# Optimization experiments

Measured on AMD Instinct MI355X. Metric: run time of the kernel, lower is better.

Reference implementation:

```python
import jax, jax.numpy as jnp
import numpy as np

B = 500000  # batch rows


def setup_inputs() -> dict:
    key = jax.random.key(0)
    k_x, k_v1, k_v2, k_l1, k_l2, k_l3 = jax.random.split(key, 6)
    return {
        "x": jax.random.normal(k_x, (B, 2), dtype=jnp.float32),
        "varphi1": jax.random.normal(k_v1, (300, 3), dtype=jnp.float32) * 0.1,
        "varphi2": jax.random.normal(k_v2, (1, 300), dtype=jnp.float32) * 0.1,
        "l1_diag": jax.random.normal(k_l1, (3,), dtype=jnp.float32),
        "l2_diag": jax.random.normal(k_l2, (300,), dtype=jnp.float32),
        "l3_diag": jax.random.normal(k_l3, (1,), dtype=jnp.float32),
    }


def reference(x, varphi1, varphi2, l1_diag, l2_diag, l3_diag):
    # append bias column of ones: [B, 3]
    xa = jnp.concatenate([x, jnp.ones((x.shape[0], 1), dtype=x.dtype)], axis=1)
    # diag(v) @ M == v[:, None] * M ; M @ diag(v) == M * v[None, :]
    W_21 = varphi1 * l1_diag[None, :] - l2_diag[:, None] * varphi1          # [300, 3]
    W_32 = varphi2 * l2_diag[None, :] - l3_diag[:, None] * varphi2          # [1, 300]
    W_31 = (l3_diag[:, None] * varphi2 - varphi2 * l2_diag[None, :]) @ varphi1  # [1, 3]
    # y = W_31 @ xa^T + W_32 @ relu(W_21 @ xa^T), returned transposed -> [B, 1]
    h = jax.nn.relu(xa @ W_21.T)                                            # [B, 300]
    y = xa @ W_31.T + h @ W_32.T                                            # [B, 1]
    return y
```

## Files before the change

kernel.cpp:

```cpp
#include <hip/hip_runtime.h>

#define NH   300
#define NPAD 320
#define BLK  256
#define RPT  8


__global__ __launch_bounds__(NPAD)
void phi2_precompute(const float* __restrict__ varphi1,
                     const float* __restrict__ varphi2,
                     const float* __restrict__ l1,
                     const float* __restrict__ l2,
                     const float* __restrict__ l3,
                     float4* __restrict__ coef,
                     float* __restrict__ w31p) {
    __shared__ float red[NPAD/64][3];
    int j = threadIdx.x;
    float p0 = 0.f, p1 = 0.f, p2 = 0.f;
    if (j < NH) {
        float lv2  = l2[j];
        float phi2 = varphi2[j];
        float W32  = phi2 * (lv2 - l3[0]);
        float s    = 0.5f * W32;
        float v0 = varphi1[j*3+0], v1 = varphi1[j*3+1], v2 = varphi1[j*3+2];
        float a = v0 * (l1[0] - lv2);
        float b = v1 * (l1[1] - lv2);
        float c = v2 * (l1[2] - lv2);
        float asafe = (fabsf(a) > 1e-20f) ? a : copysignf(1e-20f, a);
        coef[j] = make_float4(b / asafe, c / asafe, s * fabsf(asafe), 0.f);
        p0 = W32 * (0.5f * a - v0);
        p1 = W32 * (0.5f * b - v1);
        p2 = W32 * (0.5f * c - v2);
    } else {
        coef[j] = make_float4(0.f, 0.f, 0.f, 0.f);
    }
    for (int off = 32; off > 0; off >>= 1) {
        p0 += __shfl_down(p0, off);
        p1 += __shfl_down(p1, off);
        p2 += __shfl_down(p2, off);
    }
    int wave = threadIdx.x >> 6;
    if ((threadIdx.x & 63) == 0) {
        red[wave][0] = p0; red[wave][1] = p1; red[wave][2] = p2;
    }
    __syncthreads();
    if (threadIdx.x == 0) {
        float s0 = 0.f, s1 = 0.f, s2 = 0.f;
        for (int w = 0; w < NPAD/64; ++w) { s0 += red[w][0]; s1 += red[w][1]; s2 += red[w][2]; }
        w31p[0] = s0; w31p[1] = s1; w31p[2] = s2;
    }
}

__device__ __forceinline__ float rl(float v, int lane) {
    return __uint_as_float(__builtin_amdgcn_readlane(__float_as_uint(v), lane));
}

__global__ __launch_bounds__(BLK)
void phi2_main(const float* __restrict__ x,
               const float4* __restrict__ coef,
               const float* __restrict__ w31p,
               float* __restrict__ y,
               int nthreads) {
    int t    = blockIdx.x * BLK + threadIdx.x;
    int lane = threadIdx.x & 63;
    bool active = (t < nthreads);
    int tc = active ? t : (nthreads - 1);

    const float4* xq = (const float4*)x + (size_t)tc * 4;
    float4 xa = xq[0], xb = xq[1], xc = xq[2], xd = xq[3];
    float X0[RPT] = {xa.x, xa.z, xb.x, xb.z, xc.x, xc.z, xd.x, xd.z};
    float X1[RPT] = {xa.y, xa.w, xb.y, xb.w, xc.y, xc.w, xd.y, xd.w};

    float w0 = w31p[0], w1 = w31p[1], w2 = w31p[2];
    float acc[RPT];
#pragma unroll
    for (int r = 0; r < RPT; ++r)
        acc[r] = fmaf(w0, X0[r], fmaf(w1, X1[r], w2));

    float4 cur = coef[lane];
#pragma unroll
    for (int ch = 0; ch < 4; ++ch) {
        float4 nxt = coef[(ch + 1) * 64 + lane];
#pragma unroll 4
        for (int jj = 0; jj < 64; ++jj) {
            float Bv = rl(cur.x, jj);
            float Cv = rl(cur.y, jj);
            float Av = rl(cur.z, jj);
#pragma unroll
            for (int r = 0; r < RPT; ++r) {
                float tt = fmaf(Bv, X1[r], X0[r]) + Cv;
                acc[r] = fmaf(Av, fabsf(tt), acc[r]);
            }
        }
        cur = nxt;
    }
#pragma unroll 4
    for (int jj = 0; jj < 44; ++jj) {
        float Bv = rl(cur.x, jj);
        float Cv = rl(cur.y, jj);
        float Av = rl(cur.z, jj);
#pragma unroll
        for (int r = 0; r < RPT; ++r) {
            float tt = fmaf(Bv, X1[r], X0[r]) + Cv;
            acc[r] = fmaf(Av, fabsf(tt), acc[r]);
        }
    }

    if (active) {
        float4* yq = (float4*)y + (size_t)t * 2;
        yq[0] = make_float4(acc[0], acc[1], acc[2], acc[3]);
        yq[1] = make_float4(acc[4], acc[5], acc[6], acc[7]);
    }
}

extern "C" void kernel_launch(void* const* d_in, const int* in_sizes, int n_in,
                              void* d_out, int out_size, void* d_ws, size_t ws_size,
                              hipStream_t stream) {
    const float* x       = (const float*)d_in[0];
    const float* varphi1 = (const float*)d_in[1];
    const float* varphi2 = (const float*)d_in[2];
    const float* l1      = (const float*)d_in[3];
    const float* l2      = (const float*)d_in[4];
    const float* l3      = (const float*)d_in[5];

    float4* coef = (float4*)d_ws;
    float*  w31p = (float*)((char*)d_ws + NPAD * sizeof(float4));
    float*  y    = (float*)d_out;

    int B = in_sizes[0] / 2;

    phi2_precompute<<<1, NPAD, 0, stream>>>(varphi1, varphi2, l1, l2, l3, coef, w31p);

    int nthreads = (B + RPT - 1) / RPT;
    int grid = (nthreads + BLK - 1) / BLK;
    phi2_main<<<grid, BLK, 0, stream>>>(x, coef, w31p, y, nthreads);
}
```

Baseline: 83.92 us.

## Fuse coefficient precompute into main kernel, computing per-wave coefficients redundantly

Drops the separate single-block precompute kernel. Each 64-thread wave now recomputes the 300 hidden-unit coefficients in registers (5 per lane) and reduces the W31 terms with wave shuffles before running the same readlane-broadcast inner loop. This removes one kernel launch, the serialization between the two kernels, and the global round trip for the coefficients. In exchange every wave repeats the small precompute, including divisions, and the block size shrinks from 256 to 64 threads.

```diff
diff --git a/kernel.cpp b/kernel.cpp
--- a/kernel.cpp
+++ b/kernel.cpp
@@ -1,108 +1,82 @@
 #include <hip/hip_runtime.h>
 
-#define NH   300
-#define NPAD 320
-#define BLK  256
-#define RPT  8
+#define NH  300
+#define BLK 64
+#define RPT 8
 
+__device__ __forceinline__ float rl(float v, int lane) {
+    return __uint_as_float(__builtin_amdgcn_readlane(__float_as_uint(v), lane));
+}
 
-__global__ __launch_bounds__(NPAD)
-void phi2_precompute(const float* __restrict__ varphi1,
-                     const float* __restrict__ varphi2,
-                     const float* __restrict__ l1,
-                     const float* __restrict__ l2,
-                     const float* __restrict__ l3,
-                     float4* __restrict__ coef,
-                     float* __restrict__ w31p) {
-    __shared__ float red[NPAD/64][3];
-    int j = threadIdx.x;
+__global__ __launch_bounds__(BLK)
+void phi2_fused(const float* __restrict__ x,
+                const float* __restrict__ varphi1,
+                const float* __restrict__ varphi2,
+                const float* __restrict__ l1,
+                const float* __restrict__ l2,
+                const float* __restrict__ l3,
+                float* __restrict__ y,
+                int nthreads) {
+    int lane = threadIdx.x;
+    int t    = blockIdx.x * BLK + lane;
+    bool active = (t < nthreads);
+    int tc = active ? t : (nthreads - 1);
+
+    const float4* xq = (const float4*)x + (size_t)tc * 4;
+    float4 xa = xq[0], xb = xq[1], xc = xq[2], xd = xq[3];
+
+    float l10 = l1[0], l11 = l1[1], l12 = l1[2], l30 = l3[0];
+    float Bc[5], Cc[5], Ac[5];
     float p0 = 0.f, p1 = 0.f, p2 = 0.f;
-    if (j < NH) {
-        float lv2  = l2[j];
-        float phi2 = varphi2[j];
-        float W32  = phi2 * (lv2 - l3[0]);
+#pragma unroll
+    for (int ch = 0; ch < 5; ++ch) {
+        int j = ch * 64 + lane;
+        bool live = (j < NH);
+        int jc = live ? j : (NH - 1);
+        float lv2  = l2[jc];
+        float phi2 = varphi2[jc];
+        float W32  = live ? phi2 * (lv2 - l30) : 0.f;
         float s    = 0.5f * W32;
-        float v0 = varphi1[j*3+0], v1 = varphi1[j*3+1], v2 = varphi1[j*3+2];
-        float a = v0 * (l1[0] - lv2);
-        float b = v1 * (l1[1] - lv2);
-        float c = v2 * (l1[2] - lv2);
+        float v0 = varphi1[jc*3+0], v1 = varphi1[jc*3+1], v2 = varphi1[jc*3+2];
+        float a = v0 * (l10 - lv2);
+        float b = v1 * (l11 - lv2);
+        float c = v2 * (l12 - lv2);
         float asafe = (fabsf(a) > 1e-20f) ? a : copysignf(1e-20f, a);
-        coef[j] = make_float4(b / asafe, c / asafe, s * fabsf(asafe), 0.f);
-        p0 = W32 * (0.5f * a - v0);
-        p1 = W32 * (0.5f * b - v1);
-        p2 = W32 * (0.5f * c - v2);
-    } else {
-        coef[j] = make_float4(0.f, 0.f, 0.f, 0.f);
+        float inva  = 1.0f / asafe;
+        Bc[ch] = b * inva;
+        Cc[ch] = c * inva;
+        Ac[ch] = s * fabsf(asafe);
+        p0 = fmaf(W32, 0.5f * a - v0, p0);
+        p1 = fmaf(W32, 0.5f * b - v1, p1);
+        p2 = fmaf(W32, 0.5f * c - v2, p2);
     }
     for (int off = 32; off > 0; off >>= 1) {
         p0 += __shfl_down(p0, off);
         p1 += __shfl_down(p1, off);
         p2 += __shfl_down(p2, off);
     }
-    int wave = threadIdx.x >> 6;
-    if ((threadIdx.x & 63) == 0) {
-        red[wave][0] = p0; red[wave][1] = p1; red[wave][2] = p2;
-    }
-    __syncthreads();
-    if (threadIdx.x == 0) {
-        float s0 = 0.f, s1 = 0.f, s2 = 0.f;
-        for (int w = 0; w < NPAD/64; ++w) { s0 += red[w][0]; s1 += red[w][1]; s2 += red[w][2]; }
-        w31p[0] = s0; w31p[1] = s1; w31p[2] = s2;
-    }
-}
+    p0 = rl(p0, 0); p1 = rl(p1, 0); p2 = rl(p2, 0);
 
-__device__ __forceinline__ float rl(float v, int lane) {
-    return __uint_as_float(__builtin_amdgcn_readlane(__float_as_uint(v), lane));
-}
-
-__global__ __launch_bounds__(BLK)
-void phi2_main(const float* __restrict__ x,
-               const float4* __restrict__ coef,
-               const float* __restrict__ w31p,
-               float* __restrict__ y,
-               int nthreads) {
-    int t    = blockIdx.x * BLK + threadIdx.x;
-    int lane = threadIdx.x & 63;
-    bool active = (t < nthreads);
-    int tc = active ? t : (nthreads - 1);
-
-    const float4* xq = (const float4*)x + (size_t)tc * 4;
-    float4 xa = xq[0], xb = xq[1], xc = xq[2], xd = xq[3];
     float X0[RPT] = {xa.x, xa.z, xb.x, xb.z, xc.x, xc.z, xd.x, xd.z};
     float X1[RPT] = {xa.y, xa.w, xb.y, xb.w, xc.y, xc.w, xd.y, xd.w};
-
-    float w0 = w31p[0], w1 = w31p[1], w2 = w31p[2];
     float acc[RPT];
 #pragma unroll
     for (int r = 0; r < RPT; ++r)
-        acc[r] = fmaf(w0, X0[r], fmaf(w1, X1[r], w2));
+        acc[r] = fmaf(p0, X0[r], fmaf(p1, X1[r], p2));
 
-    float4 cur = coef[lane];
 #pragma unroll
-    for (int ch = 0; ch < 4; ++ch) {
-        float4 nxt = coef[(ch + 1) * 64 + lane];
+    for (int ch = 0; ch < 5; ++ch) {
+        const int cnt = (ch == 4) ? (NH - 256) : 64;
 #pragma unroll 4
-        for (int jj = 0; jj < 64; ++jj) {
-            float Bv = rl(cur.x, jj);
-            float Cv = rl(cur.y, jj);
-            float Av = rl(cur.z, jj);
+        for (int jj = 0; jj < cnt; ++jj) {
+            float Bs = rl(Bc[ch], jj);
+            float Cs = rl(Cc[ch], jj);
+            float As = rl(Ac[ch], jj);
 #pragma unroll
             for (int r = 0; r < RPT; ++r) {
-                float tt = fmaf(Bv, X1[r], X0[r]) + Cv;
-                acc[r] = fmaf(Av, fabsf(tt), acc[r]);
+                float tt = fmaf(Bs, X1[r], X0[r]) + Cs;
+                acc[r] = fmaf(As, fabsf(tt), acc[r]);
             }
-        }
-        cur = nxt;
-    }
-#pragma unroll 4
-    for (int jj = 0; jj < 44; ++jj) {
-        float Bv = rl(cur.x, jj);
-        float Cv = rl(cur.y, jj);
-        float Av = rl(cur.z, jj);
-#pragma unroll
-        for (int r = 0; r < RPT; ++r) {
-            float tt = fmaf(Bv, X1[r], X0[r]) + Cv;
-            acc[r] = fmaf(Av, fabsf(tt), acc[r]);
         }
     }
 
@@ -122,16 +96,11 @@
     const float* l1      = (const float*)d_in[3];
     const float* l2      = (const float*)d_in[4];
     const float* l3      = (const float*)d_in[5];
-
-    float4* coef = (float4*)d_ws;
-    float*  w31p = (float*)((char*)d_ws + NPAD * sizeof(float4));
-    float*  y    = (float*)d_out;
+    float*       y       = (float*)d_out;
 
     int B = in_sizes[0] / 2;
-
-    phi2_precompute<<<1, NPAD, 0, stream>>>(varphi1, varphi2, l1, l2, l3, coef, w31p);
-
     int nthreads = (B + RPT - 1) / RPT;
     int grid = (nthreads + BLK - 1) / BLK;
-    phi2_main<<<grid, BLK, 0, stream>>>(x, coef, w31p, y, nthreads);
+
+    phi2_fused<<<grid, BLK, 0, stream>>>(x, varphi1, varphi2, l1, l2, l3, y, nthreads);
 }
```

After: 83.14 us. About the same (-0.9%).
